# Optimization experiments

Hardware: AMD Instinct MI355X
Metric: run time of the kernel (lower is better)

Reference implementation:

```python
import jax, jax.numpy as jnp
import numpy as np

B, H, W, C = 32, 56, 56, 256
WS, SHIFT, HEADS = 7, 3, 8
N = WS * WS
EPS = 1e-5


def _rel_pos_index(ws):
    coords = np.stack(np.meshgrid(np.arange(ws), np.arange(ws), indexing='ij'))  # [2,ws,ws]
    flat = coords.reshape(2, -1)
    rel = flat[:, :, None] - flat[:, None, :]            # [2,N,N]
    rel = rel.transpose(1, 2, 0)
    rel[:, :, 0] += ws - 1
    rel[:, :, 1] += ws - 1
    rel[:, :, 0] *= 2 * ws - 1
    return rel.sum(-1)                                    # [N,N] int


def _attn_mask(h, w, ws, shift):
    img = np.zeros((h, w))
    slices = (slice(0, -ws), slice(-ws, -shift), slice(-shift, None))
    cnt = 0
    for hs in slices:
        for wsl in slices:
            img[hs, wsl] = cnt
            cnt += 1
    mw = img.reshape(h // ws, ws, w // ws, ws).transpose(0, 2, 1, 3).reshape(-1, ws * ws)
    d = mw[:, None, :] - mw[:, :, None]
    return np.where(d != 0, -100.0, 0.0).astype(np.float32)  # [nW,N,N]


REL_IDX = jnp.asarray(_rel_pos_index(WS))
ATTN_MASK = jnp.asarray(_attn_mask(H, W, WS, SHIFT))


def layer_norm(x, g, b):
    m = jnp.mean(x, -1, keepdims=True)
    v = jnp.mean(jnp.square(x - m), -1, keepdims=True)
    return (x - m) * jax.lax.rsqrt(v + EPS) * g + b


def window_partition(x, ws):
    b, h, w, c = x.shape
    x = x.reshape(b, h // ws, ws, w // ws, ws, c)
    return x.transpose(0, 1, 3, 2, 4, 5).reshape(-1, ws, ws, c)


def window_reverse(win, ws, h, w):
    b = win.shape[0] // ((h // ws) * (w // ws))
    x = win.reshape(b, h // ws, w // ws, ws, ws, -1)
    return x.transpose(0, 1, 3, 2, 4, 5).reshape(b, h, w, -1)


def setup_inputs() -> dict:
    key = jax.random.key(0)
    ks = jax.random.split(key, 8)
    s = lambda fan: 1.0 / np.sqrt(fan)
    return {
        'x': jax.random.normal(ks[0], (B, H * W, C), jnp.float32),
        'ln1_g': jnp.ones((C,), jnp.float32),
        'ln1_b': jnp.zeros((C,), jnp.float32),
        'dw_w': jax.random.normal(ks[1], (3, 3, 1, C), jnp.float32) * s(9),
        'dw_b': jnp.zeros((C,), jnp.float32),
        'qkv_w': jax.random.normal(ks[2], (3 * C, C), jnp.float32) * s(C),
        'qkv_b': jnp.zeros((3 * C,), jnp.float32),
        'rpb_table': jax.random.normal(ks[3], (169, HEADS), jnp.float32) * 0.02,
        'proj_w': jax.random.normal(ks[4], (C, C), jnp.float32) * s(C),
        'proj_b': jnp.zeros((C,), jnp.float32),
        'ln2_g': jnp.ones((C,), jnp.float32),
        'ln2_b': jnp.zeros((C,), jnp.float32),
        'mlp_w1': jax.random.normal(ks[5], (4 * C, C), jnp.float32) * s(C),
        'mlp_b1': jnp.zeros((4 * C,), jnp.float32),
        'mlp_w2': jax.random.normal(ks[6], (4 * C, 4 * C), jnp.float32) * s(4 * C),
        'mlp_b2': jnp.zeros((4 * C,), jnp.float32),
        'mlp_w3': jax.random.normal(ks[7], (C, 4 * C), jnp.float32) * s(4 * C),
        'mlp_b3': jnp.zeros((C,), jnp.float32),
    }


def reference(x, ln1_g, ln1_b, dw_w, dw_b, qkv_w, qkv_b, rpb_table, proj_w,
              proj_b, ln2_g, ln2_b, mlp_w1, mlp_b1, mlp_w2, mlp_b2, mlp_w3, mlp_b3):
    shortcut = x
    xn = layer_norm(x, ln1_g, ln1_b)                      # [B,L,C]
    xi = xn.reshape(B, H, W, C)

    # local enhancement: depthwise 3x3 conv (groups=C)
    x_local = jax.lax.conv_general_dilated(
        xi, dw_w, (1, 1), 'SAME',
        dimension_numbers=('NHWC', 'HWIO', 'NHWC'), feature_group_count=C) + dw_b
    x_local = x_local.reshape(B, H * W, C)

    # cyclic shift + window partition
    shifted = jnp.roll(xi, (-SHIFT, -SHIFT), axis=(1, 2))
    win = window_partition(shifted, WS).reshape(-1, N, C)  # [B*nW,N,C]
    B_ = win.shape[0]
    hd = C // HEADS

    qkv = win @ qkv_w.T + qkv_b                            # [B_,N,3C]
    qkv = qkv.reshape(B_, N, 3, HEADS, hd).transpose(2, 0, 3, 1, 4)
    q, k, v = qkv[0], qkv[1], qkv[2]                       # [B_,h,N,d]
    attn = jnp.einsum('bhnd,bhmd->bhnm', q * (hd ** -0.5), k)

    bias = rpb_table[REL_IDX.reshape(-1)].reshape(N, N, HEADS).transpose(2, 0, 1)
    attn = attn + bias[None]

    nW = ATTN_MASK.shape[0]
    attn = attn.reshape(B_ // nW, nW, HEADS, N, N) + ATTN_MASK[None, :, None]
    attn = jax.nn.softmax(attn.reshape(B_, HEADS, N, N), axis=-1)

    out = jnp.einsum('bhnm,bhmd->bhnd', attn, v).transpose(0, 2, 1, 3).reshape(B_, N, C)
    out = out @ proj_w.T + proj_b

    out = window_reverse(out.reshape(-1, WS, WS, C), WS, H, W)
    out = jnp.roll(out, (SHIFT, SHIFT), axis=(1, 2)).reshape(B, H * W, C)

    x = shortcut + out + 0.1 * x_local

    h1 = jax.nn.gelu(layer_norm(x, ln2_g, ln2_b) @ mlp_w1.T + mlp_b1, approximate=False)
    h2 = jax.nn.gelu(h1 @ mlp_w2.T + mlp_b2, approximate=False)
    x = x + (h2 @ mlp_w3.T + mlp_b3)
    return x
```

## Files before the change

kernel.cpp:

```cpp
#include <hip/hip_runtime.h>
#include <cstdio>
#include <cstdlib>

#define DEVI __device__ __forceinline__

typedef __bf16 bf16_8 __attribute__((ext_vector_type(8)));
typedef float f32x4 __attribute__((ext_vector_type(4)));

DEVI float b2f(unsigned short u){ unsigned int x=((unsigned int)u)<<16; float f; __builtin_memcpy(&f,&x,sizeof(f)); return f; }
DEVI unsigned short f2b(float f){ unsigned int u; __builtin_memcpy(&u,&f,sizeof(u)); u = u + 0x7fffu + ((u>>16)&1u); return (unsigned short)(u>>16); }
DEVI float gelu_f(float x){ return 0.5f*x*(1.0f+erff(x*0.70710678118654752f)); }

DEVI void gload16(const unsigned short* g, unsigned short* l){
  __builtin_amdgcn_global_load_lds((const __attribute__((address_space(1))) void*)g,
                                   (__attribute__((address_space(3))) void*)l, 16, 0, 0);
}

DEVI int win_row_to_pixel(int row){
  int win = row / 49;
  int pos = row - win*49;
  int b  = win >> 6, wi = win & 63;
  int ph = pos / 7,  pw = pos - ph*7;
  int sh = (wi>>3)*7 + ph, sw = (wi&7)*7 + pw;
  int h = sh + 3; if (h >= 56) h -= 56;
  int w = sw + 3; if (w >= 56) w -= 56;
  return b*3136 + h*56 + w;
}

template<int K, int EPI>
__global__ __launch_bounds__(256)
void gemm_k(const unsigned short* __restrict__ A, const unsigned short* __restrict__ Bw,
            const float* __restrict__ bias, void* __restrict__ outp,
            const float* __restrict__ aux0, const unsigned short* __restrict__ aux1,
            int am0, int om0)
{
  __shared__ unsigned short As[2][128*64];
  __shared__ unsigned short Bs[2][128*64];
  const int tid = threadIdx.x;
  const int wave = tid >> 6, lane = tid & 63;
  const int tn = blockIdx.x, tm = blockIdx.y;
  const int g = lane >> 4, c = lane & 15;

  const unsigned short* ap[4];
  const unsigned short* bp[4];
  {
    int coff = (lane & 7) * 8;
    int rb = wave*32 + (lane >> 3);
#pragma unroll
    for (int j = 0; j < 4; j++){
      int r = rb + j*8;
      int am = am0 + tm*128 + r;
      int arow = (EPI == 0) ? win_row_to_pixel(am) : am;
      ap[j] = A  + (size_t)arow * K + coff;
      bp[j] = Bw + (size_t)(tn*128 + r) * K + coff;
    }
  }
  const f32x4 z4 = {0.f,0.f,0.f,0.f};
  f32x4 acc[4][4];
#pragma unroll
  for (int mi=0;mi<4;mi++)
#pragma unroll
    for (int ni=0;ni<4;ni++) acc[mi][ni] = z4;

  const int wr = wave >> 1, wc = wave & 1;
  const int ldsoff = wave*2048;

#pragma unroll
  for (int j=0;j<4;j++){
    gload16(ap[j], &As[0][ldsoff + j*512]);
    gload16(bp[j], &Bs[0][ldsoff + j*512]);
  }
  __syncthreads();

  constexpr int NK = K/64;
  int cur = 0;
  for (int ks=0; ks<NK; ks++){
    if (ks+1 < NK){
      int k0 = (ks+1)*64;
#pragma unroll
      for (int j=0;j<4;j++){
        gload16(ap[j]+k0, &As[cur^1][ldsoff + j*512]);
        gload16(bp[j]+k0, &Bs[cur^1][ldsoff + j*512]);
      }
    }
#pragma unroll
    for (int kk=0;kk<2;kk++){
      bf16_8 af[4], bfr[4];
#pragma unroll
      for (int mi=0;mi<4;mi++) af[mi]  = *(const bf16_8*)&As[cur][(wr*64+mi*16+c)*64 + kk*32 + g*8];
#pragma unroll
      for (int ni=0;ni<4;ni++) bfr[ni] = *(const bf16_8*)&Bs[cur][(wc*64+ni*16+c)*64 + kk*32 + g*8];
#pragma unroll
      for (int mi=0;mi<4;mi++)
#pragma unroll
        for (int ni=0;ni<4;ni++)
          acc[mi][ni] = __builtin_amdgcn_mfma_f32_16x16x32_bf16(af[mi], bfr[ni], acc[mi][ni], 0,0,0);
    }
    __syncthreads();
    cur ^= 1;
  }

  const int N = gridDim.x * 128;
#pragma unroll
  for (int mi=0;mi<4;mi++){
#pragma unroll
    for (int r=0;r<4;r++){
      int lrow = tm*128 + wr*64 + mi*16 + g*4 + r;
      int pix = 0;
      if constexpr (EPI == 1) pix = win_row_to_pixel(om0 + lrow);
#pragma unroll
      for (int ni=0;ni<4;ni++){
        int col = tn*128 + wc*64 + ni*16 + c;
        float v = acc[mi][ni][r] + bias[col];
        if constexpr (EPI == 0){
          ((unsigned short*)outp)[(size_t)lrow*768 + col] = f2b(v);
        } else if constexpr (EPI == 1){
          size_t idx = (size_t)pix*256 + col;
          ((float*)outp)[idx] = v + aux0[idx] + 0.1f*b2f(aux1[idx]);
        } else if constexpr (EPI == 2){
          ((unsigned short*)outp)[(size_t)lrow*N + col] = f2b(gelu_f(v));
        } else {
          size_t idx = (size_t)(om0 + lrow)*256 + col;
          ((float*)outp)[idx] = v + aux0[idx];
        }
      }
    }
  }
}

__global__ __launch_bounds__(512)
void attn_kernel(const unsigned short* __restrict__ qkv, const float* __restrict__ rpb,
                 unsigned short* __restrict__ out, int win_base)
{
  __shared__ unsigned int KV[8][49*16*2];
  const int lwin = blockIdx.x;
  const int head = threadIdx.x >> 6, lane = threadIdx.x & 63;
  const int wi = (win_base + lwin) & 63, wh = wi >> 3, ww = wi & 7;
  const unsigned short* base = qkv + (size_t)lwin*49*768 + head*32;

  for (int i = lane; i < 49*16; i += 64){
    int m = i >> 4, d2 = i & 15;
    KV[head][i]       = *(const unsigned int*)(base + 256 + (size_t)m*768 + d2*2);
    KV[head][784 + i] = *(const unsigned int*)(base + 512 + (size_t)m*768 + d2*2);
  }
  __syncthreads();
  const int n = lane;
  if (n >= 49) return;

  float q[32];
#pragma unroll
  for (int d2 = 0; d2 < 16; d2++){
    unsigned int u = *(const unsigned int*)(base + (size_t)n*768 + d2*2);
    q[d2*2]   = b2f((unsigned short)(u & 0xffffu));
    q[d2*2+1] = b2f((unsigned short)(u >> 16));
  }
  const int yn = n/7, xq = n - (n/7)*7;
  const int syn = wh*7+yn, sxn = ww*7+xq;
  const int regn = ((syn<49)?0:((syn<53)?1:2))*3 + ((sxn<49)?0:((sxn<53)?1:2));
  const float scale = 0.17677669529663687f;

  float p[49]; float mx = -1e30f;
#pragma unroll
  for (int m = 0; m < 49; m++){
    float s = 0.f;
#pragma unroll
    for (int d2 = 0; d2 < 16; d2++){
      unsigned int u = KV[head][m*16 + d2];
      s += q[d2*2]   * b2f((unsigned short)(u & 0xffffu));
      s += q[d2*2+1] * b2f((unsigned short)(u >> 16));
    }
    int ym = m/7, xm = m - (m/7)*7;
    int sym = wh*7+ym, sxm = ww*7+xm;
    int regm = ((sym<49)?0:((sym<53)?1:2))*3 + ((sxm<49)?0:((sxm<53)?1:2));
    float v = s*scale + rpb[((yn-ym+6)*13 + (xq-xm+6))*8 + head]
            + ((regn!=regm) ? -100.f : 0.f);
    p[m] = v; mx = fmaxf(mx, v);
  }
  float sum = 0.f;
#pragma unroll
  for (int m = 0; m < 49; m++){ p[m] = __expf(p[m]-mx); sum += p[m]; }
  const float inv = 1.0f/sum;

  float o[32];
#pragma unroll
  for (int d = 0; d < 32; d++) o[d] = 0.f;
#pragma unroll
  for (int m = 0; m < 49; m++){
    float pm = p[m]*inv;
#pragma unroll
    for (int d2 = 0; d2 < 16; d2++){
      unsigned int u = KV[head][784 + m*16 + d2];
      o[d2*2]   += pm * b2f((unsigned short)(u & 0xffffu));
      o[d2*2+1] += pm * b2f((unsigned short)(u >> 16));
    }
  }
  size_t ob = ((size_t)lwin*49 + n)*256 + head*32;
#pragma unroll
  for (int d2 = 0; d2 < 16; d2++){
    unsigned int w = (unsigned int)f2b(o[d2*2]) | ((unsigned int)f2b(o[d2*2+1])<<16);
    *(unsigned int*)&out[ob + d2*2] = w;
  }
}

__global__ __launch_bounds__(256)
void ln_kernel(const float* __restrict__ x, const float* __restrict__ gw,
               const float* __restrict__ bw, unsigned short* __restrict__ out)
{
  const int wave = threadIdx.x >> 6, lane = threadIdx.x & 63;
  const size_t row = (size_t)blockIdx.x*4 + wave;
  const float4 v = *(const float4*)&x[row*256 + lane*4];
  float s = v.x+v.y+v.z+v.w;
  float q = v.x*v.x+v.y*v.y+v.z*v.z+v.w*v.w;
#pragma unroll
  for (int m=1;m<64;m<<=1){ s += __shfl_xor(s,m); q += __shfl_xor(q,m); }
  float mean = s*(1.0f/256.0f);
  float var  = q*(1.0f/256.0f) - mean*mean;
  float rstd = rsqrtf(var + 1e-5f);
  const float4 gg = *(const float4*)&gw[lane*4];
  const float4 bb = *(const float4*)&bw[lane*4];
  unsigned int lo = (unsigned int)f2b((v.x-mean)*rstd*gg.x + bb.x)
                  | ((unsigned int)f2b((v.y-mean)*rstd*gg.y + bb.y) << 16);
  unsigned int hi = (unsigned int)f2b((v.z-mean)*rstd*gg.z + bb.z)
                  | ((unsigned int)f2b((v.w-mean)*rstd*gg.w + bb.w) << 16);
  *(uint2*)&out[row*256 + lane*4] = make_uint2(lo, hi);
}

__global__ __launch_bounds__(256)
void dwconv_kernel(const unsigned short* __restrict__ xn, const float* __restrict__ w,
                   const float* __restrict__ bias, unsigned short* __restrict__ out)
{
  int idx = blockIdx.x*256 + threadIdx.x;
  int c4  = idx & 63;
  int t   = idx >> 6;
  int b   = t / 3136;
  int pix = t - b*3136;
  int h = pix / 56, wq = pix - h*56;
  float4 acc = *(const float4*)&bias[c4*4];
#pragma unroll
  for (int ky=0;ky<3;ky++){
    int hy = h + ky - 1;
    if ((unsigned)hy >= 56u) continue;
#pragma unroll
    for (int kx=0;kx<3;kx++){
      int wx = wq + kx - 1;
      if ((unsigned)wx >= 56u) continue;
      const uint2 raw = *(const uint2*)&xn[(((size_t)b*3136 + hy*56 + wx)<<8) + c4*4];
      const float4 wv = *(const float4*)&w[((ky*3+kx)<<8) + c4*4];
      acc.x += b2f((unsigned short)(raw.x & 0xffffu)) * wv.x;
      acc.y += b2f((unsigned short)(raw.x >> 16))     * wv.y;
      acc.z += b2f((unsigned short)(raw.y & 0xffffu)) * wv.z;
      acc.w += b2f((unsigned short)(raw.y >> 16))     * wv.w;
    }
  }
  unsigned int lo = (unsigned int)f2b(acc.x) | ((unsigned int)f2b(acc.y)<<16);
  unsigned int hi = (unsigned int)f2b(acc.z) | ((unsigned int)f2b(acc.w)<<16);
  *(uint2*)&out[(size_t)idx*4] = make_uint2(lo,hi);
}

__global__ void cvt_kernel(const float* __restrict__ in, unsigned short* __restrict__ out, int n4)
{
  int i = blockIdx.x*256 + threadIdx.x;
  if (i < n4){
    float4 v = ((const float4*)in)[i];
    unsigned int lo = (unsigned int)f2b(v.x) | ((unsigned int)f2b(v.y)<<16);
    unsigned int hi = (unsigned int)f2b(v.z) | ((unsigned int)f2b(v.w)<<16);
    ((uint2*)out)[i] = make_uint2(lo,hi);
  }
}

extern "C" void kernel_launch(void* const* d_in, const int* in_sizes, int n_in,
                              void* d_out, int out_size, void* d_ws, size_t ws_size,
                              hipStream_t stream)
{
  (void)in_sizes; (void)n_in; (void)out_size;
  const float* x     = (const float*)d_in[0];
  const float* ln1g  = (const float*)d_in[1];
  const float* ln1b  = (const float*)d_in[2];
  const float* dww   = (const float*)d_in[3];
  const float* dwb   = (const float*)d_in[4];
  const float* qkvw  = (const float*)d_in[5];
  const float* qkvb  = (const float*)d_in[6];
  const float* rpb   = (const float*)d_in[7];
  const float* projw = (const float*)d_in[8];
  const float* projb = (const float*)d_in[9];
  const float* ln2g  = (const float*)d_in[10];
  const float* ln2b  = (const float*)d_in[11];
  const float* w1    = (const float*)d_in[12];
  const float* b1    = (const float*)d_in[13];
  const float* w2    = (const float*)d_in[14];
  const float* b2    = (const float*)d_in[15];
  const float* w3    = (const float*)d_in[16];
  const float* b3    = (const float*)d_in[17];

  char* ws = (char*)d_ws;
  constexpr size_t OFF_XN = 3670016;
  constexpr size_t OFF_XL = OFF_XN + 51380224;
  constexpr size_t OFF_S  = OFF_XL + 51380224;
  int CH = 6272;
  if      (ws_size >= OFF_S + 100352ull*4096) CH = 100352;
  else if (ws_size >= OFF_S + 50176ull*4096)  CH = 50176;
  else if (ws_size >= OFF_S + 25088ull*2048)  CH = 25088;
  else if (ws_size >= OFF_S + 12544ull*2048)  CH = 12544;
  const int NC = 100352 / CH;

  unsigned short* wqkv = (unsigned short*)(ws + 0);
  unsigned short* wproj= wqkv + 196608;
  unsigned short* wm1  = wproj + 65536;
  unsigned short* wm2  = wm1 + 262144;
  unsigned short* wm3  = wm2 + 1048576;
  unsigned short* xn   = (unsigned short*)(ws + OFF_XN);
  unsigned short* xl   = (unsigned short*)(ws + OFF_XL);
  unsigned short* qkvc = (unsigned short*)(ws + OFF_S);
  unsigned short* aoc  = (unsigned short*)(ws + OFF_S + (size_t)CH*1536);
  unsigned short* h2c  = (unsigned short*)(ws + OFF_S);
  unsigned short* h1c  = (CH <= 25088) ? (unsigned short*)(ws + OFF_XL)
                                       : (unsigned short*)(ws + OFF_S + (size_t)CH*2048);
  float* x2 = (float*)d_out;

  cvt_kernel<<<192,  256, 0, stream>>>(qkvw,  wqkv,  49152);
  cvt_kernel<<<64,   256, 0, stream>>>(projw, wproj, 16384);
  cvt_kernel<<<256,  256, 0, stream>>>(w1,    wm1,   65536);
  cvt_kernel<<<1024, 256, 0, stream>>>(w2,    wm2,   262144);
  cvt_kernel<<<256,  256, 0, stream>>>(w3,    wm3,   65536);

  ln_kernel<<<25088, 256, 0, stream>>>(x, ln1g, ln1b, xn);
  dwconv_kernel<<<25088, 256, 0, stream>>>(xn, dww, dwb, xl);

  for (int cch = 0; cch < NC; ++cch){
    int m0 = cch * CH;
    gemm_k<256,0><<<dim3(6, CH/128), 256, 0, stream>>>(xn, wqkv, qkvb, qkvc, nullptr, nullptr, m0, 0);
    attn_kernel<<<CH/49, 512, 0, stream>>>(qkvc, rpb, aoc, m0/49);
    gemm_k<256,1><<<dim3(2, CH/128), 256, 0, stream>>>(aoc, wproj, projb, x2, x, xl, 0, m0);
  }

  ln_kernel<<<25088, 256, 0, stream>>>(x2, ln2g, ln2b, xn);

  for (int cch = 0; cch < NC; ++cch){
    int m0 = cch * CH;
    gemm_k<256,2> <<<dim3(8, CH/128), 256, 0, stream>>>(xn,  wm1, b1, h1c, nullptr, nullptr, m0, 0);
    gemm_k<1024,2><<<dim3(8, CH/128), 256, 0, stream>>>(h1c, wm2, b2, h2c, nullptr, nullptr, 0, 0);
    gemm_k<1024,3><<<dim3(2, CH/128), 256, 0, stream>>>(h2c, wm3, b3, x2, x2, nullptr, 0, m0);
  }
}
```

Baseline: 1.812 ms.

## Swizzle GEMM tile order, recompute attention scores, fix chunk size

The GEMM kernel remaps each block's linear index so that consecutive blocks are spread across 8 interleaved chunks. The aim is better L2 and cache locality across XCDs. The attention kernel drops the 49-element score array: it computes the max and sum with an online softmax, then recomputes the QK scores in the PV loop, and the loops are no longer unrolled. This cuts register pressure to raise occupancy, at the cost of doing the dot products twice. The chunk size is now fixed at 25088 rows instead of being picked from the workspace size, which assumes the workspace is large enough.

```diff
diff --git a/kernel.cpp b/kernel.cpp
--- a/kernel.cpp
+++ b/kernel.cpp
@@ -27,7 +27,7 @@
   return b*3136 + h*56 + w;
 }
 
-template<int K, int EPI>
+template<int K, int EPI, int NX>
 __global__ __launch_bounds__(256)
 void gemm_k(const unsigned short* __restrict__ A, const unsigned short* __restrict__ Bw,
             const float* __restrict__ bias, void* __restrict__ outp,
@@ -38,7 +38,10 @@
   __shared__ unsigned short Bs[2][128*64];
   const int tid = threadIdx.x;
   const int wave = tid >> 6, lane = tid & 63;
-  const int tn = blockIdx.x, tm = blockIdx.y;
+  const int L = blockIdx.y * NX + blockIdx.x;
+  const int chunk = (NX * gridDim.y) >> 3;
+  const int swz = (L & 7) * chunk + (L >> 3);
+  const int tm = swz / NX, tn = swz - tm * NX;
   const int g = lane >> 4, c = lane & 15;
 
   const unsigned short* ap[4];
@@ -100,7 +103,6 @@
     cur ^= 1;
   }
 
-  const int N = gridDim.x * 128;
 #pragma unroll
   for (int mi=0;mi<4;mi++){
 #pragma unroll
@@ -118,7 +120,7 @@
           size_t idx = (size_t)pix*256 + col;
           ((float*)outp)[idx] = v + aux0[idx] + 0.1f*b2f(aux1[idx]);
         } else if constexpr (EPI == 2){
-          ((unsigned short*)outp)[(size_t)lrow*N + col] = f2b(gelu_f(v));
+          ((unsigned short*)outp)[(size_t)lrow*(NX*128) + col] = f2b(gelu_f(v));
         } else {
           size_t idx = (size_t)(om0 + lrow)*256 + col;
           ((float*)outp)[idx] = v + aux0[idx];
@@ -159,8 +161,7 @@
   const int regn = ((syn<49)?0:((syn<53)?1:2))*3 + ((sxn<49)?0:((sxn<53)?1:2));
   const float scale = 0.17677669529663687f;
 
-  float p[49]; float mx = -1e30f;
-#pragma unroll
+  float mx = -1e30f, sum = 0.f;
   for (int m = 0; m < 49; m++){
     float s = 0.f;
 #pragma unroll
@@ -174,19 +175,29 @@
     int regm = ((sym<49)?0:((sym<53)?1:2))*3 + ((sxm<49)?0:((sxm<53)?1:2));
     float v = s*scale + rpb[((yn-ym+6)*13 + (xq-xm+6))*8 + head]
             + ((regn!=regm) ? -100.f : 0.f);
-    p[m] = v; mx = fmaxf(mx, v);
-  }
-  float sum = 0.f;
-#pragma unroll
-  for (int m = 0; m < 49; m++){ p[m] = __expf(p[m]-mx); sum += p[m]; }
+    float nm = fmaxf(mx, v);
+    sum = sum*__expf(mx - nm) + __expf(v - nm);
+    mx = nm;
+  }
   const float inv = 1.0f/sum;
 
   float o[32];
 #pragma unroll
   for (int d = 0; d < 32; d++) o[d] = 0.f;
-#pragma unroll
   for (int m = 0; m < 49; m++){
-    float pm = p[m]*inv;
+    float s = 0.f;
+#pragma unroll
+    for (int d2 = 0; d2 < 16; d2++){
+      unsigned int u = KV[head][m*16 + d2];
+      s += q[d2*2]   * b2f((unsigned short)(u & 0xffffu));
+      s += q[d2*2+1] * b2f((unsigned short)(u >> 16));
+    }
+    int ym = m/7, xm = m - (m/7)*7;
+    int sym = wh*7+ym, sxm = ww*7+xm;
+    int regm = ((sym<49)?0:((sym<53)?1:2))*3 + ((sxm<49)?0:((sxm<53)?1:2));
+    float v = s*scale + rpb[((yn-ym+6)*13 + (xq-xm+6))*8 + head]
+            + ((regn!=regm) ? -100.f : 0.f);
+    float pm = __expf(v - mx);
 #pragma unroll
     for (int d2 = 0; d2 < 16; d2++){
       unsigned int u = KV[head][784 + m*16 + d2];
@@ -197,7 +208,7 @@
   size_t ob = ((size_t)lwin*49 + n)*256 + head*32;
 #pragma unroll
   for (int d2 = 0; d2 < 16; d2++){
-    unsigned int w = (unsigned int)f2b(o[d2*2]) | ((unsigned int)f2b(o[d2*2+1])<<16);
+    unsigned int w = (unsigned int)f2b(o[d2*2]*inv) | ((unsigned int)f2b(o[d2*2+1]*inv)<<16);
     *(unsigned int*)&out[ob + d2*2] = w;
   }
 }
@@ -272,7 +283,7 @@
                               void* d_out, int out_size, void* d_ws, size_t ws_size,
                               hipStream_t stream)
 {
-  (void)in_sizes; (void)n_in; (void)out_size;
+  (void)in_sizes; (void)n_in; (void)out_size; (void)ws_size;
   const float* x     = (const float*)d_in[0];
   const float* ln1g  = (const float*)d_in[1];
   const float* ln1b  = (const float*)d_in[2];
@@ -296,12 +307,8 @@
   constexpr size_t OFF_XN = 3670016;
   constexpr size_t OFF_XL = OFF_XN + 51380224;
   constexpr size_t OFF_S  = OFF_XL + 51380224;
-  int CH = 6272;
-  if      (ws_size >= OFF_S + 100352ull*4096) CH = 100352;
-  else if (ws_size >= OFF_S + 50176ull*4096)  CH = 50176;
-  else if (ws_size >= OFF_S + 25088ull*2048)  CH = 25088;
-  else if (ws_size >= OFF_S + 12544ull*2048)  CH = 12544;
-  const int NC = 100352 / CH;
+  constexpr int CH = 25088;
+  constexpr int NC = 100352 / CH;
 
   unsigned short* wqkv = (unsigned short*)(ws + 0);
   unsigned short* wproj= wqkv + 196608;
@@ -313,8 +320,7 @@
   unsigned short* qkvc = (unsigned short*)(ws + OFF_S);
   unsigned short* aoc  = (unsigned short*)(ws + OFF_S + (size_t)CH*1536);
   unsigned short* h2c  = (unsigned short*)(ws + OFF_S);
-  unsigned short* h1c  = (CH <= 25088) ? (unsigned short*)(ws + OFF_XL)
-                                       : (unsigned short*)(ws + OFF_S + (size_t)CH*2048);
+  unsigned short* h1c  = (unsigned short*)(ws + OFF_XL);
   float* x2 = (float*)d_out;
 
   cvt_kernel<<<192,  256, 0, stream>>>(qkvw,  wqkv,  49152);
@@ -328,17 +334,17 @@
 
   for (int cch = 0; cch < NC; ++cch){
     int m0 = cch * CH;
-    gemm_k<256,0><<<dim3(6, CH/128), 256, 0, stream>>>(xn, wqkv, qkvb, qkvc, nullptr, nullptr, m0, 0);
+    gemm_k<256,0,6><<<dim3(6, CH/128), 256, 0, stream>>>(xn, wqkv, qkvb, qkvc, nullptr, nullptr, m0, 0);
     attn_kernel<<<CH/49, 512, 0, stream>>>(qkvc, rpb, aoc, m0/49);
-    gemm_k<256,1><<<dim3(2, CH/128), 256, 0, stream>>>(aoc, wproj, projb, x2, x, xl, 0, m0);
+    gemm_k<256,1,2><<<dim3(2, CH/128), 256, 0, stream>>>(aoc, wproj, projb, x2, x, xl, 0, m0);
   }
 
   ln_kernel<<<25088, 256, 0, stream>>>(x2, ln2g, ln2b, xn);
 
   for (int cch = 0; cch < NC; ++cch){
     int m0 = cch * CH;
-    gemm_k<256,2> <<<dim3(8, CH/128), 256, 0, stream>>>(xn,  wm1, b1, h1c, nullptr, nullptr, m0, 0);
-    gemm_k<1024,2><<<dim3(8, CH/128), 256, 0, stream>>>(h1c, wm2, b2, h2c, nullptr, nullptr, 0, 0);
-    gemm_k<1024,3><<<dim3(2, CH/128), 256, 0, stream>>>(h2c, wm3, b3, x2, x2, nullptr, 0, m0);
-  }
-}
+    gemm_k<256,2,8> <<<dim3(8, CH/128), 256, 0, stream>>>(xn,  wm1, b1, h1c, nullptr, nullptr, m0, 0);
+    gemm_k<1024,2,8><<<dim3(8, CH/128), 256, 0, stream>>>(h1c, wm2, b2, h2c, nullptr, nullptr, 0, 0);
+    gemm_k<1024,3,2><<<dim3(2, CH/128), 256, 0, stream>>>(h2c, wm3, b3, x2, x2, nullptr, 0, m0);
+  }
+}
```

New measurement: 1.775 ms. 2.1% less time.
